# Kernel tuning notes

Hardware: AMD Instinct MI355X
Metric: run time of the kernel (lower is better)

Reference implementation:

```python
import jax, jax.numpy as jnp
import numpy as np


def setup_inputs() -> dict:
    key = jax.random.key(0)
    k1, k2, k3, k4 = jax.random.split(key, 4)
    bs, c, h, w = 8, 64, 64, 64
    x = jax.random.normal(k1, (bs, c, h, w), dtype=jnp.float32)
    # 1x1 conv weights (bias=False): stored as [out_ch, in_ch]
    wq = jax.random.normal(k2, (c // 2, c), dtype=jnp.float32) * (1.0 / np.sqrt(c))
    wk = jax.random.normal(k3, (c // 2, c), dtype=jnp.float32) * (1.0 / np.sqrt(c))
    wv = jax.random.normal(k4, (c, c), dtype=jnp.float32) * (1.0 / np.sqrt(c))
    return {"x": x, "wq": wq, "wk": wk, "wv": wv}


def reference(x, wq, wk, wv):
    bs, c, h, w = x.shape
    hw = h * w
    xf = x.reshape(bs, c, hw)  # [bs, c, hw]
    # 1x1 convs == per-position matmuls
    q = jnp.einsum('dc,bcn->bnd', wq, xf)   # [bs, hw, c//2]
    k = jnp.einsum('dc,bcn->bdn', wk, xf)   # [bs, c//2, hw]
    v = jnp.einsum('dc,bcn->bdn', wv, xf)   # [bs, c,    hw]
    energy = jnp.einsum('bnd,bdm->bnm', q, k)          # [bs, hw, hw]
    attention = jax.nn.softmax(energy, axis=-1)
    # dropout(p=0.1) is identity in eval mode
    out = jnp.einsum('bcm,bnm->bcn', v, attention)      # [bs, c, hw]
    return out.reshape(bs, c, h, w)
```

## Files before the change

### kernel.cpp

```cpp
#include <hip/hip_runtime.h>
#include <hip/hip_fp16.h>


typedef short          f16x8 __attribute__((ext_vector_type(8)));
typedef float          f32x4 __attribute__((ext_vector_type(4)));
typedef unsigned short u16;
typedef unsigned int   u32;

#define HW  4096
#define CC  64
#define DQK 32
#define NBLK2 256
#define THR2 11.54f

__device__ __forceinline__ u16 f2h(float f) {
    __half h = __float2half(f);
    return *reinterpret_cast<u16*>(&h);
}
__device__ __forceinline__ u32 pk2(float a, float b) {
    auto r = __builtin_amdgcn_cvt_pkrtz(a, b);
    u32 u; __builtin_memcpy(&u, &r, 4); return u;
}
__device__ __forceinline__ float ex2(float x) {
    return __builtin_amdgcn_exp2f(x);
}
__device__ __forceinline__ float max16(const f32x4* s) {
    float a = fmaxf(fmaxf(s[0][0], s[0][1]), s[0][2]);
    a = fmaxf(fmaxf(a, s[0][3]), s[1][0]);
    a = fmaxf(fmaxf(a, s[1][1]), s[1][2]);
    a = fmaxf(fmaxf(a, s[1][3]), s[2][0]);
    a = fmaxf(fmaxf(a, s[2][1]), s[2][2]);
    a = fmaxf(fmaxf(a, s[2][3]), s[3][0]);
    a = fmaxf(fmaxf(a, s[3][1]), s[3][2]);
    return fmaxf(a, s[3][3]);
}

__global__ __launch_bounds__(256) void proj_kernel(
    const float* __restrict__ x,  const float* __restrict__ wq,
    const float* __restrict__ wk, const float* __restrict__ wv,
    u16* __restrict__ Qr, u16* __restrict__ Kr, u16* __restrict__ Vc)
{
    const int b   = blockIdx.x;
    const int n0  = blockIdx.y * 64;
    const int tid = threadIdx.x;

    __shared__ __align__(16) u16 Xt[64][88];

    {
        const int c  = tid >> 2;
        const int nc = (tid & 3) * 16;
        const float* src = x + ((size_t)(b * CC + c) * HW + n0 + nc);
        float fv[16];
        *(f32x4*)(fv)      = *(const f32x4*)(src);
        *(f32x4*)(fv + 4)  = *(const f32x4*)(src + 4);
        *(f32x4*)(fv + 8)  = *(const f32x4*)(src + 8);
        *(f32x4*)(fv + 12) = *(const f32x4*)(src + 12);
        #pragma unroll
        for (int i = 0; i < 16; ++i) Xt[nc + i][c] = f2h(fv[i]);
    }
    __syncthreads();

    const int wave = tid >> 6;
    const int lane = tid & 63;
    const int lr   = lane & 15;
    const int lg   = lane >> 4;
    const int lk   = lg * 8;

    const float* W = (wave == 0) ? wq : (wave == 1) ? wk
                   : (wave == 2) ? wv : (wv + 32 * 64);
    const float scale = (wave == 0) ? 1.4426950408889634f : 1.0f;

    f16x8 a[2][2];
    #pragma unroll
    for (int dt = 0; dt < 2; ++dt)
        #pragma unroll
        for (int h = 0; h < 2; ++h) {
            const float* p = W + (dt * 16 + lr) * 64 + h * 32 + lk;
            f32x4 lo = *(const f32x4*)p, hi = *(const f32x4*)(p + 4);
            u16 t[8];
            #pragma unroll
            for (int j = 0; j < 4; ++j) {
                t[j]     = f2h(lo[j] * scale);
                t[4 + j] = f2h(hi[j] * scale);
            }
            a[dt][h] = *(const f16x8*)t;
        }

    const f32x4 fz = {0.f, 0.f, 0.f, 0.f};
    f32x4 acc[2][4];
    #pragma unroll
    for (int dt = 0; dt < 2; ++dt)
        #pragma unroll
        for (int nt = 0; nt < 4; ++nt) acc[dt][nt] = fz;

    #pragma unroll
    for (int nt = 0; nt < 4; ++nt)
        #pragma unroll
        for (int h = 0; h < 2; ++h) {
            f16x8 bx = *(const f16x8*)(&Xt[nt * 16 + lr][h * 32 + lk]);
            #pragma unroll
            for (int dt = 0; dt < 2; ++dt)
                acc[dt][nt] = __builtin_amdgcn_mfma_f32_16x16x32_f16(
                                  a[dt][h], bx, acc[dt][nt], 0, 0, 0);
        }

    if (wave < 2) {
        u16* Out = (wave == 0) ? Qr : Kr;
        #pragma unroll
        for (int dt = 0; dt < 2; ++dt)
            #pragma unroll
            for (int nt = 0; nt < 4; ++nt) {
                const int n = n0 + nt * 16 + lr;
                const int d = dt * 16 + lg * 4;
                u16 pkk[4];
                #pragma unroll
                for (int r = 0; r < 4; ++r) pkk[r] = f2h(acc[dt][nt][r]);
                *(uint2*)(Out + ((size_t)(b * HW + n) * DQK + d)) = *(uint2*)pkk;
            }
    } else {
        const int cbase = (wave - 2) * 32;
        #pragma unroll
        for (int dt = 0; dt < 2; ++dt)
            #pragma unroll
            for (int nt = 0; nt < 4; ++nt) {
                const int m = n0 + nt * 16 + lr;
                #pragma unroll
                for (int r = 0; r < 4; ++r) {
                    const int c = cbase + dt * 16 + lg * 4 + r;
                    Vc[(size_t)(b * CC + c) * HW + m] = f2h(acc[dt][nt][r]);
                }
            }
    }
}

template<int S>
__global__ __launch_bounds__(256, 4) void attn_kernel(
    const u16* __restrict__ Qr, const u16* __restrict__ Kr,
    const u16* __restrict__ Vc, float* __restrict__ out,
    float* __restrict__ Opart, float* __restrict__ Ml)
{
    const int b    = blockIdx.x;
    const int nb   = blockIdx.y;
    const int sp   = blockIdx.z;
    const int n0   = nb * 128;
    const int tid  = threadIdx.x;
    const int wave = tid >> 6;
    const int lane = tid & 63;
    const int lr   = lane & 15;
    const int lg   = lane >> 4;
    const int lk   = lg * 8;

    __shared__ __align__(16) u16 K_lds[2][64 * 40];
    __shared__ __align__(16) u16 V_lds[2][64 * 72];

    const int qb = n0 + wave * 32;
    const f16x8 aq0 = *(const f16x8*)(Qr + (size_t)(b * HW + qb + lr) * DQK + lk);
    const f16x8 aq1 = *(const f16x8*)(Qr + (size_t)(b * HW + qb + 16 + lr) * DQK + lk);

    const f16x8 ones = { 0x3C00, 0x3C00, 0x3C00, 0x3C00,
                         0x3C00, 0x3C00, 0x3C00, 0x3C00 };
    const f32x4 fz = {0.f, 0.f, 0.f, 0.f};

    const int km = tid >> 2, kc = tid & 3;
    const int krow = (km & 32) | (((km >> 2) & 1) << 4)
                   | (((km >> 3) & 3) << 2) | (km & 3);
    const int c0 = tid >> 3, ch = tid & 7;
    const int c1 = 32 + c0;

    const int kvbase = sp * (HW / S);
    const int NT     = HW / S / 64;

    const u16* Kb  = Kr + (size_t)(b * HW + kvbase + km) * DQK + kc * 8;
    const u16* Vb0 = Vc + (size_t)(b * CC + c0) * HW + kvbase + ch * 8;
    const u16* Vb1 = Vc + (size_t)(b * CC + c1) * HW + kvbase + ch * 8;

    f16x8 kreg  = *(const f16x8*)(Kb);
    f16x8 v0reg = *(const f16x8*)(Vb0);
    f16x8 v1reg = *(const f16x8*)(Vb1);
    *(f16x8*)&K_lds[0][krow * 40 + kc * 8] = kreg;
    *(f16x8*)&V_lds[0][c0 * 72 + ch * 8]   = v0reg;
    *(f16x8*)&V_lds[0][c1 * 72 + ch * 8]   = v1reg;
    if (NT > 1) {
        kreg  = *(const f16x8*)(Kb  + (size_t)64 * DQK);
        v0reg = *(const f16x8*)(Vb0 + 64);
        v1reg = *(const f16x8*)(Vb1 + 64);
    }

    f32x4 o[2][4];
    #pragma unroll
    for (int qs = 0; qs < 2; ++qs)
        #pragma unroll
        for (int ct = 0; ct < 4; ++ct) o[qs][ct] = fz;
    f32x4 lrow[2] = {fz, fz};
    float mrow[2] = {-1e30f, -1e30f};

    for (int t = 0; t < NT; ++t) {
        __syncthreads();
        const int cur = t & 1;
        const u16* Kc = K_lds[cur];
        const u16* Vcur = V_lds[cur];

        f32x4 s0[4], s1[4];
        #pragma unroll
        for (int mt = 0; mt < 4; ++mt) {
            f16x8 kf = *(const f16x8*)&Kc[(mt * 16 + lr) * 40 + lk];
            s0[mt] = __builtin_amdgcn_mfma_f32_16x16x32_f16(kf, aq0, fz, 0, 0, 0);
            s1[mt] = __builtin_amdgcn_mfma_f32_16x16x32_f16(kf, aq1, fz, 0, 0, 0);
        }

        if (t + 1 < NT) {
            const int nxt = cur ^ 1;
            *(f16x8*)&K_lds[nxt][krow * 40 + kc * 8] = kreg;
            *(f16x8*)&V_lds[nxt][c0 * 72 + ch * 8]   = v0reg;
            *(f16x8*)&V_lds[nxt][c1 * 72 + ch * 8]   = v1reg;
            if (t + 2 < NT) {
                kreg  = *(const f16x8*)(Kb  + (size_t)(t + 2) * 64 * DQK);
                v0reg = *(const f16x8*)(Vb0 + (t + 2) * 64);
                v1reg = *(const f16x8*)(Vb1 + (t + 2) * 64);
            }
        }

        float lm0 = max16(s0);
        float lm1 = max16(s1);
        if (__any((lm0 > mrow[0] + THR2) | (lm1 > mrow[1] + THR2))) {
            #pragma unroll
            for (int qs = 0; qs < 2; ++qs) {
                float v = qs ? lm1 : lm0;
                v = fmaxf(v, __shfl_xor(v, 16, 64));
                v = fmaxf(v, __shfl_xor(v, 32, 64));
                float mnew  = fmaxf(mrow[qs], v);
                float alpha = ex2(mrow[qs] - mnew);
                mrow[qs] = mnew;
                f32x4 al;
                #pragma unroll
                for (int r = 0; r < 4; ++r) al[r] = __shfl(alpha, 4 * lg + r, 64);
                #pragma unroll
                for (int ct = 0; ct < 4; ++ct)
                    #pragma unroll
                    for (int r = 0; r < 4; ++r) o[qs][ct][r] *= al[r];
                #pragma unroll
                for (int r = 0; r < 4; ++r) lrow[qs][r] *= al[r];
            }
        }

        f16x8 pa[2][2];
        #pragma unroll
        for (int qs = 0; qs < 2; ++qs) {
            const float m = mrow[qs];
            #pragma unroll
            for (int h = 0; h < 2; ++h) {
                u32 w[4];
                #pragma unroll
                for (int half = 0; half < 2; ++half) {
                    const f32x4& sv = qs ? s1[2 * h + half] : s0[2 * h + half];
                    float p0 = ex2(sv[0] - m), p1 = ex2(sv[1] - m);
                    float p2 = ex2(sv[2] - m), p3 = ex2(sv[3] - m);
                    w[2 * half]     = pk2(p0, p1);
                    w[2 * half + 1] = pk2(p2, p3);
                }
                __builtin_memcpy(&pa[qs][h], w, 16);
            }
        }

        #pragma unroll
        for (int qs = 0; qs < 2; ++qs) {
            f32x4 rs = __builtin_amdgcn_mfma_f32_16x16x32_f16(pa[qs][0], ones, fz, 0, 0, 0);
            rs = __builtin_amdgcn_mfma_f32_16x16x32_f16(pa[qs][1], ones, rs, 0, 0, 0);
            #pragma unroll
            for (int r = 0; r < 4; ++r) lrow[qs][r] += rs[r];
        }

        #pragma unroll
        for (int ct = 0; ct < 4; ++ct) {
            const int c = ct * 16 + lr;
            f16x8 bv0 = *(const f16x8*)&Vcur[c * 72 + lk];
            f16x8 bv1 = *(const f16x8*)&Vcur[c * 72 + 32 + lk];
            o[0][ct] = __builtin_amdgcn_mfma_f32_16x16x32_f16(pa[0][0], bv0, o[0][ct], 0, 0, 0);
            o[0][ct] = __builtin_amdgcn_mfma_f32_16x16x32_f16(pa[0][1], bv1, o[0][ct], 0, 0, 0);
            o[1][ct] = __builtin_amdgcn_mfma_f32_16x16x32_f16(pa[1][0], bv0, o[1][ct], 0, 0, 0);
            o[1][ct] = __builtin_amdgcn_mfma_f32_16x16x32_f16(pa[1][1], bv1, o[1][ct], 0, 0, 0);
        }
    }

    if constexpr (S == 1) {
        #pragma unroll
        for (int qs = 0; qs < 2; ++qs)
            #pragma unroll
            for (int ct = 0; ct < 4; ++ct) {
                const int c = ct * 16 + lr;
                f32x4 st;
                #pragma unroll
                for (int r = 0; r < 4; ++r) st[r] = o[qs][ct][r] / lrow[qs][r];
                *(f32x4*)(out + (size_t)(b * CC + c) * HW + qb + qs * 16 + lg * 4) = st;
            }
    } else {
        const int bnb = b * 32 + nb;
        float* Op = Opart + ((size_t)(sp * NBLK2 + bnb) * 64) * 128;
        #pragma unroll
        for (int qs = 0; qs < 2; ++qs)
            #pragma unroll
            for (int ct = 0; ct < 4; ++ct) {
                const int c    = ct * 16 + lr;
                const int qloc = wave * 32 + qs * 16 + lg * 4;
                *(f32x4*)(Op + (size_t)c * 128 + qloc) = o[qs][ct];
            }
        float* Mp = Ml + (size_t)(sp * NBLK2 + bnb) * 256;
        if (lg == 0) {
            Mp[wave * 32 + lr]      = mrow[0];
            Mp[wave * 32 + 16 + lr] = mrow[1];
        }
        if (lr == 0) {
            #pragma unroll
            for (int qs = 0; qs < 2; ++qs)
                #pragma unroll
                for (int r = 0; r < 4; ++r)
                    Mp[128 + wave * 32 + qs * 16 + 4 * lg + r] = lrow[qs][r];
        }
    }
}

template<int S>
__global__ __launch_bounds__(256) void combine_kernel(
    const float* __restrict__ Opart, const float* __restrict__ Ml,
    float* __restrict__ out)
{
    const int bnb = blockIdx.x;
    const int b = bnb >> 5, nb = bnb & 31;
    const int tid = threadIdx.x;
    const int c  = tid >> 2;
    const int q0 = (tid & 3) * 32;

    #pragma unroll
    for (int qq = 0; qq < 32; qq += 4) {
        const int q = q0 + qq;
        f32x4 ms[S], ls[S];
        #pragma unroll
        for (int s = 0; s < S; ++s) {
            const float* Mp = Ml + (size_t)(s * NBLK2 + bnb) * 256;
            ms[s] = *(const f32x4*)(Mp + q);
            ls[s] = *(const f32x4*)(Mp + 128 + q);
        }
        f32x4 M = ms[0];
        #pragma unroll
        for (int s = 1; s < S; ++s)
            #pragma unroll
            for (int j = 0; j < 4; ++j) M[j] = fmaxf(M[j], ms[s][j]);
        f32x4 den = {0.f, 0.f, 0.f, 0.f};
        f32x4 w[S];
        #pragma unroll
        for (int s = 0; s < S; ++s)
            #pragma unroll
            for (int j = 0; j < 4; ++j) {
                w[s][j] = __builtin_amdgcn_exp2f(ms[s][j] - M[j]);
                den[j] += ls[s][j] * w[s][j];
            }
        f32x4 acc = {0.f, 0.f, 0.f, 0.f};
        #pragma unroll
        for (int s = 0; s < S; ++s) {
            f32x4 Ov = *(const f32x4*)(Opart +
                          ((size_t)(s * NBLK2 + bnb) * 64 + c) * 128 + q);
            #pragma unroll
            for (int j = 0; j < 4; ++j) acc[j] += w[s][j] * Ov[j];
        }
        #pragma unroll
        for (int j = 0; j < 4; ++j) acc[j] /= den[j];
        *(f32x4*)(out + (size_t)(b * CC + c) * HW + nb * 128 + q) = acc;
    }
}

extern "C" void kernel_launch(void* const* d_in, const int* in_sizes, int n_in,
                              void* d_out, int out_size, void* d_ws, size_t ws_size,
                              hipStream_t stream)
{
    const float* x  = (const float*)d_in[0];
    const float* wq = (const float*)d_in[1];
    const float* wk = (const float*)d_in[2];
    const float* wv = (const float*)d_in[3];
    u16* ws  = (u16*)d_ws;
    u16* Qr  = ws;
    u16* Kr  = ws + (size_t)8 * HW * DQK;
    u16* Vc  = ws + (size_t)16 * HW * DQK;
    float* Opart = (float*)(ws + (size_t)4194304);
    float* out = (float*)d_out;

    proj_kernel<<<dim3(8, 64), 256, 0, stream>>>(x, wq, wk, wv, Qr, Kr, Vc);

    const size_t qkv_b   = 8ull * 1024 * 1024;
    const size_t opart_b = (size_t)NBLK2 * 64 * 128 * 4;
    const size_t ml_b    = (size_t)NBLK2 * 256 * 4;

    if (ws_size >= qkv_b + 4 * (opart_b + ml_b)) {
        float* Ml = Opart + 4ull * NBLK2 * 64 * 128;
        attn_kernel<4><<<dim3(8, 32, 4), 256, 0, stream>>>(Qr, Kr, Vc, out, Opart, Ml);
        combine_kernel<4><<<NBLK2, 256, 0, stream>>>(Opart, Ml, out);
    } else if (ws_size >= qkv_b + 2 * (opart_b + ml_b)) {
        float* Ml = Opart + 2ull * NBLK2 * 64 * 128;
        attn_kernel<2><<<dim3(8, 32, 2), 256, 0, stream>>>(Qr, Kr, Vc, out, Opart, Ml);
        combine_kernel<2><<<NBLK2, 256, 0, stream>>>(Opart, Ml, out);
    } else {
        attn_kernel<1><<<dim3(8, 32, 1), 256, 0, stream>>>(Qr, Kr, Vc, out, nullptr, nullptr);
    }
}
```

Measured before the change: 74.29 us.

## Store K/V in MFMA fragment order and load directly to registers, drop LDS

The projection kernel now writes K and V in a per-tile layout that matches the MFMA operand fragments. The attention kernel can then load each lane's fragments straight from global memory into registers, which removes the LDS staging, the double buffering and the per-tile __syncthreads. The loop also splits the two query sub-tiles into sequential halves, prefetching the next tile's K and V between them. Partial outputs are normalised and stored as fp16 to halve the combine traffic. The cost is redundant global/L2 loads, since every wave reads the same K/V, and some precision loss in the partials.

```diff
diff --git a/kernel.cpp b/kernel.cpp
--- a/kernel.cpp
+++ b/kernel.cpp
@@ -16,6 +16,9 @@
 __device__ __forceinline__ u16 f2h(float f) {
     __half h = __float2half(f);
     return *reinterpret_cast<u16*>(&h);
+}
+__device__ __forceinline__ float h2f(u16 u) {
+    __half h; __builtin_memcpy(&h, &u, 2); return __half2float(h);
 }
 __device__ __forceinline__ u32 pk2(float a, float b) {
     auto r = __builtin_amdgcn_cvt_pkrtz(a, b);
@@ -38,11 +41,12 @@
 __global__ __launch_bounds__(256) void proj_kernel(
     const float* __restrict__ x,  const float* __restrict__ wq,
     const float* __restrict__ wk, const float* __restrict__ wv,
-    u16* __restrict__ Qr, u16* __restrict__ Kr, u16* __restrict__ Vc)
+    u16* __restrict__ Qr, u16* __restrict__ Kf, u16* __restrict__ Vf)
 {
-    const int b   = blockIdx.x;
-    const int n0  = blockIdx.y * 64;
-    const int tid = threadIdx.x;
+    const int b    = blockIdx.x;
+    const int tile = blockIdx.y;
+    const int n0   = tile * 64;
+    const int tid  = threadIdx.x;
 
     __shared__ __align__(16) u16 Xt[64][88];
 
@@ -104,8 +108,7 @@
                                   a[dt][h], bx, acc[dt][nt], 0, 0, 0);
         }
 
-    if (wave < 2) {
-        u16* Out = (wave == 0) ? Qr : Kr;
+    if (wave == 0) {
         #pragma unroll
         for (int dt = 0; dt < 2; ++dt)
             #pragma unroll
@@ -115,7 +118,23 @@
                 u16 pkk[4];
                 #pragma unroll
                 for (int r = 0; r < 4; ++r) pkk[r] = f2h(acc[dt][nt][r]);
-                *(uint2*)(Out + ((size_t)(b * HW + n) * DQK + d)) = *(uint2*)pkk;
+                *(uint2*)(Qr + ((size_t)(b * HW + n) * DQK + d)) = *(uint2*)pkk;
+            }
+    } else if (wave == 1) {
+        #pragma unroll
+        for (int dt = 0; dt < 2; ++dt)
+            #pragma unroll
+            for (int nt = 0; nt < 4; ++nt) {
+                const int m_in = nt * 16 + lr;
+                const int mt   = 2 * (m_in >> 5) + ((m_in >> 2) & 1);
+                const int lrk  = ((m_in >> 4) & 1) * 8 + ((m_in >> 3) & 1) * 4 + (m_in & 3);
+                const int lgk  = dt * 2 + (lg >> 1);
+                const int j0   = (lg & 1) * 4;
+                u16 pkk[4];
+                #pragma unroll
+                for (int r = 0; r < 4; ++r) pkk[r] = f2h(acc[dt][nt][r]);
+                *(uint2*)(Kf + (size_t)(b * 64 + tile) * 2048
+                             + mt * 512 + lgk * 128 + lrk * 8 + j0) = *(uint2*)pkk;
             }
     } else {
         const int cbase = (wave - 2) * 32;
@@ -123,11 +142,17 @@
         for (int dt = 0; dt < 2; ++dt)
             #pragma unroll
             for (int nt = 0; nt < 4; ++nt) {
-                const int m = n0 + nt * 16 + lr;
+                const int m_in = nt * 16 + lr;
+                const int h    = m_in >> 5;
+                const int lgv  = (m_in >> 3) & 3;
+                const int j    = m_in & 7;
                 #pragma unroll
                 for (int r = 0; r < 4; ++r) {
-                    const int c = cbase + dt * 16 + lg * 4 + r;
-                    Vc[(size_t)(b * CC + c) * HW + m] = f2h(acc[dt][nt][r]);
+                    const int c  = cbase + dt * 16 + lg * 4 + r;
+                    const int ct = c >> 4, lrv = c & 15;
+                    Vf[(size_t)(b * 64 + tile) * 4096
+                       + ct * 1024 + h * 512 + lgv * 128 + lrv * 8 + j]
+                        = f2h(acc[dt][nt][r]);
                 }
             }
     }
@@ -135,14 +160,14 @@
 
 template<int S>
 __global__ __launch_bounds__(256, 4) void attn_kernel(
-    const u16* __restrict__ Qr, const u16* __restrict__ Kr,
-    const u16* __restrict__ Vc, float* __restrict__ out,
-    float* __restrict__ Opart, float* __restrict__ Ml)
+    const u16* __restrict__ Qr, const u16* __restrict__ Kf,
+    const u16* __restrict__ Vf, float* __restrict__ out,
+    u16* __restrict__ Opart, float* __restrict__ Ml)
 {
+    constexpr int NT = HW / S / 64;
     const int b    = blockIdx.x;
     const int nb   = blockIdx.y;
     const int sp   = blockIdx.z;
-    const int n0   = nb * 128;
     const int tid  = threadIdx.x;
     const int wave = tid >> 6;
     const int lane = tid & 63;
@@ -150,10 +175,7 @@
     const int lg   = lane >> 4;
     const int lk   = lg * 8;
 
-    __shared__ __align__(16) u16 K_lds[2][64 * 40];
-    __shared__ __align__(16) u16 V_lds[2][64 * 72];
-
-    const int qb = n0 + wave * 32;
+    const int qb = nb * 128 + wave * 32;
     const f16x8 aq0 = *(const f16x8*)(Qr + (size_t)(b * HW + qb + lr) * DQK + lk);
     const f16x8 aq1 = *(const f16x8*)(Qr + (size_t)(b * HW + qb + 16 + lr) * DQK + lk);
 
@@ -161,30 +183,19 @@
                          0x3C00, 0x3C00, 0x3C00, 0x3C00 };
     const f32x4 fz = {0.f, 0.f, 0.f, 0.f};
 
-    const int km = tid >> 2, kc = tid & 3;
-    const int krow = (km & 32) | (((km >> 2) & 1) << 4)
-                   | (((km >> 3) & 3) << 2) | (km & 3);
-    const int c0 = tid >> 3, ch = tid & 7;
-    const int c1 = 32 + c0;
-
-    const int kvbase = sp * (HW / S);
-    const int NT     = HW / S / 64;
-
-    const u16* Kb  = Kr + (size_t)(b * HW + kvbase + km) * DQK + kc * 8;
-    const u16* Vb0 = Vc + (size_t)(b * CC + c0) * HW + kvbase + ch * 8;
-    const u16* Vb1 = Vc + (size_t)(b * CC + c1) * HW + kvbase + ch * 8;
-
-    f16x8 kreg  = *(const f16x8*)(Kb);
-    f16x8 v0reg = *(const f16x8*)(Vb0);
-    f16x8 v1reg = *(const f16x8*)(Vb1);
-    *(f16x8*)&K_lds[0][krow * 40 + kc * 8] = kreg;
-    *(f16x8*)&V_lds[0][c0 * 72 + ch * 8]   = v0reg;
-    *(f16x8*)&V_lds[0][c1 * 72 + ch * 8]   = v1reg;
-    if (NT > 1) {
-        kreg  = *(const f16x8*)(Kb  + (size_t)64 * DQK);
-        v0reg = *(const f16x8*)(Vb0 + 64);
-        v1reg = *(const f16x8*)(Vb1 + 64);
-    }
+    const int tile0 = sp * NT;
+    const u16* KfT = Kf + (size_t)(b * 64 + tile0) * 2048 + lg * 128 + lr * 8;
+    const u16* VfT = Vf + (size_t)(b * 64 + tile0) * 4096 + lg * 128 + lr * 8;
+
+    f16x8 kf[4], vf[4][2];
+    #pragma unroll
+    for (int mt = 0; mt < 4; ++mt)
+        kf[mt] = *(const f16x8*)(KfT + mt * 512);
+    #pragma unroll
+    for (int ct = 0; ct < 4; ++ct)
+        #pragma unroll
+        for (int h = 0; h < 2; ++h)
+            vf[ct][h] = *(const f16x8*)(VfT + ct * 1024 + h * 512);
 
     f32x4 o[2][4];
     #pragma unroll
@@ -194,92 +205,114 @@
     f32x4 lrow[2] = {fz, fz};
     float mrow[2] = {-1e30f, -1e30f};
 
+    #pragma unroll 2
     for (int t = 0; t < NT; ++t) {
-        __syncthreads();
-        const int cur = t & 1;
-        const u16* Kc = K_lds[cur];
-        const u16* Vcur = V_lds[cur];
-
-        f32x4 s0[4], s1[4];
-        #pragma unroll
-        for (int mt = 0; mt < 4; ++mt) {
-            f16x8 kf = *(const f16x8*)&Kc[(mt * 16 + lr) * 40 + lk];
-            s0[mt] = __builtin_amdgcn_mfma_f32_16x16x32_f16(kf, aq0, fz, 0, 0, 0);
-            s1[mt] = __builtin_amdgcn_mfma_f32_16x16x32_f16(kf, aq1, fz, 0, 0, 0);
-        }
-
-        if (t + 1 < NT) {
-            const int nxt = cur ^ 1;
-            *(f16x8*)&K_lds[nxt][krow * 40 + kc * 8] = kreg;
-            *(f16x8*)&V_lds[nxt][c0 * 72 + ch * 8]   = v0reg;
-            *(f16x8*)&V_lds[nxt][c1 * 72 + ch * 8]   = v1reg;
-            if (t + 2 < NT) {
-                kreg  = *(const f16x8*)(Kb  + (size_t)(t + 2) * 64 * DQK);
-                v0reg = *(const f16x8*)(Vb0 + (t + 2) * 64);
-                v1reg = *(const f16x8*)(Vb1 + (t + 2) * 64);
-            }
-        }
-
-        float lm0 = max16(s0);
-        float lm1 = max16(s1);
-        if (__any((lm0 > mrow[0] + THR2) | (lm1 > mrow[1] + THR2))) {
-            #pragma unroll
-            for (int qs = 0; qs < 2; ++qs) {
-                float v = qs ? lm1 : lm0;
-                v = fmaxf(v, __shfl_xor(v, 16, 64));
-                v = fmaxf(v, __shfl_xor(v, 32, 64));
-                float mnew  = fmaxf(mrow[qs], v);
-                float alpha = ex2(mrow[qs] - mnew);
-                mrow[qs] = mnew;
-                f32x4 al;
-                #pragma unroll
-                for (int r = 0; r < 4; ++r) al[r] = __shfl(alpha, 4 * lg + r, 64);
-                #pragma unroll
-                for (int ct = 0; ct < 4; ++ct)
-                    #pragma unroll
-                    for (int r = 0; r < 4; ++r) o[qs][ct][r] *= al[r];
-                #pragma unroll
-                for (int r = 0; r < 4; ++r) lrow[qs][r] *= al[r];
-            }
-        }
-
-        f16x8 pa[2][2];
-        #pragma unroll
-        for (int qs = 0; qs < 2; ++qs) {
-            const float m = mrow[qs];
+        const int tn = (t + 1 < NT) ? t + 1 : t;
+
+        f32x4 s[4];
+        #pragma unroll
+        for (int mt = 0; mt < 4; ++mt)
+            s[mt] = __builtin_amdgcn_mfma_f32_16x16x32_f16(kf[mt], aq0, fz, 0, 0, 0);
+
+        float lm = max16(s);
+        if (__any(lm > mrow[0] + THR2)) {
+            float v = lm;
+            v = fmaxf(v, __shfl_xor(v, 16, 64));
+            v = fmaxf(v, __shfl_xor(v, 32, 64));
+            float mnew  = fmaxf(mrow[0], v);
+            float alpha = ex2(mrow[0] - mnew);
+            mrow[0] = mnew;
+            f32x4 al;
+            #pragma unroll
+            for (int r = 0; r < 4; ++r) al[r] = __shfl(alpha, 4 * lg + r, 64);
+            #pragma unroll
+            for (int ct = 0; ct < 4; ++ct)
+                #pragma unroll
+                for (int r = 0; r < 4; ++r) o[0][ct][r] *= al[r];
+            #pragma unroll
+            for (int r = 0; r < 4; ++r) lrow[0][r] *= al[r];
+        }
+        f16x8 pa0[2];
+        {
+            const float m = mrow[0];
             #pragma unroll
             for (int h = 0; h < 2; ++h) {
                 u32 w[4];
-                #pragma unroll
-                for (int half = 0; half < 2; ++half) {
-                    const f32x4& sv = qs ? s1[2 * h + half] : s0[2 * h + half];
-                    float p0 = ex2(sv[0] - m), p1 = ex2(sv[1] - m);
-                    float p2 = ex2(sv[2] - m), p3 = ex2(sv[3] - m);
-                    w[2 * half]     = pk2(p0, p1);
-                    w[2 * half + 1] = pk2(p2, p3);
-                }
-                __builtin_memcpy(&pa[qs][h], w, 16);
-            }
-        }
-
-        #pragma unroll
-        for (int qs = 0; qs < 2; ++qs) {
-            f32x4 rs = __builtin_amdgcn_mfma_f32_16x16x32_f16(pa[qs][0], ones, fz, 0, 0, 0);
-            rs = __builtin_amdgcn_mfma_f32_16x16x32_f16(pa[qs][1], ones, rs, 0, 0, 0);
-            #pragma unroll
-            for (int r = 0; r < 4; ++r) lrow[qs][r] += rs[r];
-        }
-
+                w[0] = pk2(ex2(s[2*h][0] - m), ex2(s[2*h][1] - m));
+                w[1] = pk2(ex2(s[2*h][2] - m), ex2(s[2*h][3] - m));
+                w[2] = pk2(ex2(s[2*h+1][0] - m), ex2(s[2*h+1][1] - m));
+                w[3] = pk2(ex2(s[2*h+1][2] - m), ex2(s[2*h+1][3] - m));
+                __builtin_memcpy(&pa0[h], w, 16);
+            }
+        }
+        {
+            f32x4 rs = __builtin_amdgcn_mfma_f32_16x16x32_f16(pa0[0], ones, fz, 0, 0, 0);
+            rs = __builtin_amdgcn_mfma_f32_16x16x32_f16(pa0[1], ones, rs, 0, 0, 0);
+            #pragma unroll
+            for (int r = 0; r < 4; ++r) lrow[0][r] += rs[r];
+        }
         #pragma unroll
         for (int ct = 0; ct < 4; ++ct) {
-            const int c = ct * 16 + lr;
-            f16x8 bv0 = *(const f16x8*)&Vcur[c * 72 + lk];
-            f16x8 bv1 = *(const f16x8*)&Vcur[c * 72 + 32 + lk];
-            o[0][ct] = __builtin_amdgcn_mfma_f32_16x16x32_f16(pa[0][0], bv0, o[0][ct], 0, 0, 0);
-            o[0][ct] = __builtin_amdgcn_mfma_f32_16x16x32_f16(pa[0][1], bv1, o[0][ct], 0, 0, 0);
-            o[1][ct] = __builtin_amdgcn_mfma_f32_16x16x32_f16(pa[1][0], bv0, o[1][ct], 0, 0, 0);
-            o[1][ct] = __builtin_amdgcn_mfma_f32_16x16x32_f16(pa[1][1], bv1, o[1][ct], 0, 0, 0);
-        }
+            o[0][ct] = __builtin_amdgcn_mfma_f32_16x16x32_f16(pa0[0], vf[ct][0], o[0][ct], 0, 0, 0);
+            o[0][ct] = __builtin_amdgcn_mfma_f32_16x16x32_f16(pa0[1], vf[ct][1], o[0][ct], 0, 0, 0);
+        }
+
+        #pragma unroll
+        for (int mt = 0; mt < 4; ++mt)
+            s[mt] = __builtin_amdgcn_mfma_f32_16x16x32_f16(kf[mt], aq1, fz, 0, 0, 0);
+
+        #pragma unroll
+        for (int mt = 0; mt < 4; ++mt)
+            kf[mt] = *(const f16x8*)(KfT + (size_t)tn * 2048 + mt * 512);
+
+        lm = max16(s);
+        if (__any(lm > mrow[1] + THR2)) {
+            float v = lm;
+            v = fmaxf(v, __shfl_xor(v, 16, 64));
+            v = fmaxf(v, __shfl_xor(v, 32, 64));
+            float mnew  = fmaxf(mrow[1], v);
+            float alpha = ex2(mrow[1] - mnew);
+            mrow[1] = mnew;
+            f32x4 al;
+            #pragma unroll
+            for (int r = 0; r < 4; ++r) al[r] = __shfl(alpha, 4 * lg + r, 64);
+            #pragma unroll
+            for (int ct = 0; ct < 4; ++ct)
+                #pragma unroll
+                for (int r = 0; r < 4; ++r) o[1][ct][r] *= al[r];
+            #pragma unroll
+            for (int r = 0; r < 4; ++r) lrow[1][r] *= al[r];
+        }
+        f16x8 pa1[2];
+        {
+            const float m = mrow[1];
+            #pragma unroll
+            for (int h = 0; h < 2; ++h) {
+                u32 w[4];
+                w[0] = pk2(ex2(s[2*h][0] - m), ex2(s[2*h][1] - m));
+                w[1] = pk2(ex2(s[2*h][2] - m), ex2(s[2*h][3] - m));
+                w[2] = pk2(ex2(s[2*h+1][0] - m), ex2(s[2*h+1][1] - m));
+                w[3] = pk2(ex2(s[2*h+1][2] - m), ex2(s[2*h+1][3] - m));
+                __builtin_memcpy(&pa1[h], w, 16);
+            }
+        }
+        {
+            f32x4 rs = __builtin_amdgcn_mfma_f32_16x16x32_f16(pa1[0], ones, fz, 0, 0, 0);
+            rs = __builtin_amdgcn_mfma_f32_16x16x32_f16(pa1[1], ones, rs, 0, 0, 0);
+            #pragma unroll
+            for (int r = 0; r < 4; ++r) lrow[1][r] += rs[r];
+        }
+        #pragma unroll
+        for (int ct = 0; ct < 4; ++ct) {
+            o[1][ct] = __builtin_amdgcn_mfma_f32_16x16x32_f16(pa1[0], vf[ct][0], o[1][ct], 0, 0, 0);
+            o[1][ct] = __builtin_amdgcn_mfma_f32_16x16x32_f16(pa1[1], vf[ct][1], o[1][ct], 0, 0, 0);
+        }
+
+        #pragma unroll
+        for (int ct = 0; ct < 4; ++ct)
+            #pragma unroll
+            for (int h = 0; h < 2; ++h)
+                vf[ct][h] = *(const f16x8*)(VfT + (size_t)tn * 4096 + ct * 1024 + h * 512);
     }
 
     if constexpr (S == 1) {
@@ -295,14 +328,17 @@
             }
     } else {
         const int bnb = b * 32 + nb;
-        float* Op = Opart + ((size_t)(sp * NBLK2 + bnb) * 64) * 128;
+        u16* Op = Opart + ((size_t)(sp * NBLK2 + bnb) * 64) * 128;
         #pragma unroll
         for (int qs = 0; qs < 2; ++qs)
             #pragma unroll
             for (int ct = 0; ct < 4; ++ct) {
                 const int c    = ct * 16 + lr;
                 const int qloc = wave * 32 + qs * 16 + lg * 4;
-                *(f32x4*)(Op + (size_t)c * 128 + qloc) = o[qs][ct];
+                u16 pkk[4];
+                #pragma unroll
+                for (int r = 0; r < 4; ++r) pkk[r] = f2h(o[qs][ct][r] / lrow[qs][r]);
+                *(uint2*)(Op + (size_t)c * 128 + qloc) = *(uint2*)pkk;
             }
         float* Mp = Ml + (size_t)(sp * NBLK2 + bnb) * 256;
         if (lg == 0) {
@@ -321,7 +357,7 @@
 
 template<int S>
 __global__ __launch_bounds__(256) void combine_kernel(
-    const float* __restrict__ Opart, const float* __restrict__ Ml,
+    const u16* __restrict__ Opart, const float* __restrict__ Ml,
     float* __restrict__ out)
 {
     const int bnb = blockIdx.x;
@@ -333,34 +369,38 @@
     #pragma unroll
     for (int qq = 0; qq < 32; qq += 4) {
         const int q = q0 + qq;
-        f32x4 ms[S], ls[S];
+        f32x4 wl[S];
+        f32x4 den = {0.f, 0.f, 0.f, 0.f};
+        f32x4 M;
+        {
+            f32x4 ms[S], ls[S];
+            #pragma unroll
+            for (int s = 0; s < S; ++s) {
+                const float* Mp = Ml + (size_t)(s * NBLK2 + bnb) * 256;
+                ms[s] = *(const f32x4*)(Mp + q);
+                ls[s] = *(const f32x4*)(Mp + 128 + q);
+            }
+            M = ms[0];
+            #pragma unroll
+            for (int s = 1; s < S; ++s)
+                #pragma unroll
+                for (int j = 0; j < 4; ++j) M[j] = fmaxf(M[j], ms[s][j]);
+            #pragma unroll
+            for (int s = 0; s < S; ++s)
+                #pragma unroll
+                for (int j = 0; j < 4; ++j) {
+                    wl[s][j] = ex2(ms[s][j] - M[j]) * ls[s][j];
+                    den[j] += wl[s][j];
+                }
+        }
+        f32x4 acc = {0.f, 0.f, 0.f, 0.f};
         #pragma unroll
         for (int s = 0; s < S; ++s) {
-            const float* Mp = Ml + (size_t)(s * NBLK2 + bnb) * 256;
-            ms[s] = *(const f32x4*)(Mp + q);
-            ls[s] = *(const f32x4*)(Mp + 128 + q);
-        }
-        f32x4 M = ms[0];
-        #pragma unroll
-        for (int s = 1; s < S; ++s)
-            #pragma unroll
-            for (int j = 0; j < 4; ++j) M[j] = fmaxf(M[j], ms[s][j]);
-        f32x4 den = {0.f, 0.f, 0.f, 0.f};
-        f32x4 w[S];
-        #pragma unroll
-        for (int s = 0; s < S; ++s)
-            #pragma unroll
-            for (int j = 0; j < 4; ++j) {
-                w[s][j] = __builtin_amdgcn_exp2f(ms[s][j] - M[j]);
-                den[j] += ls[s][j] * w[s][j];
-            }
-        f32x4 acc = {0.f, 0.f, 0.f, 0.f};
-        #pragma unroll
-        for (int s = 0; s < S; ++s) {
-            f32x4 Ov = *(const f32x4*)(Opart +
+            uint2 hv = *(const uint2*)(Opart +
                           ((size_t)(s * NBLK2 + bnb) * 64 + c) * 128 + q);
-            #pragma unroll
-            for (int j = 0; j < 4; ++j) acc[j] += w[s][j] * Ov[j];
+            u16 h4[4]; __builtin_memcpy(h4, &hv, 8);
+            #pragma unroll
+            for (int j = 0; j < 4; ++j) acc[j] += wl[s][j] * h2f(h4[j]);
         }
         #pragma unroll
         for (int j = 0; j < 4; ++j) acc[j] /= den[j];
@@ -378,26 +418,26 @@
     const float* wv = (const float*)d_in[3];
     u16* ws  = (u16*)d_ws;
     u16* Qr  = ws;
-    u16* Kr  = ws + (size_t)8 * HW * DQK;
-    u16* Vc  = ws + (size_t)16 * HW * DQK;
-    float* Opart = (float*)(ws + (size_t)4194304);
+    u16* Kf  = ws + (size_t)8 * HW * DQK;
+    u16* Vf  = ws + (size_t)16 * HW * DQK;
+    u16* Opart = ws + (size_t)4194304;
     float* out = (float*)d_out;
 
-    proj_kernel<<<dim3(8, 64), 256, 0, stream>>>(x, wq, wk, wv, Qr, Kr, Vc);
+    proj_kernel<<<dim3(8, 64), 256, 0, stream>>>(x, wq, wk, wv, Qr, Kf, Vf);
 
     const size_t qkv_b   = 8ull * 1024 * 1024;
-    const size_t opart_b = (size_t)NBLK2 * 64 * 128 * 4;
+    const size_t opart_b = (size_t)NBLK2 * 64 * 128 * 2;
     const size_t ml_b    = (size_t)NBLK2 * 256 * 4;
 
     if (ws_size >= qkv_b + 4 * (opart_b + ml_b)) {
-        float* Ml = Opart + 4ull * NBLK2 * 64 * 128;
-        attn_kernel<4><<<dim3(8, 32, 4), 256, 0, stream>>>(Qr, Kr, Vc, out, Opart, Ml);
+        float* Ml = (float*)(Opart + 4ull * NBLK2 * 64 * 128);
+        attn_kernel<4><<<dim3(8, 32, 4), 256, 0, stream>>>(Qr, Kf, Vf, out, Opart, Ml);
         combine_kernel<4><<<NBLK2, 256, 0, stream>>>(Opart, Ml, out);
     } else if (ws_size >= qkv_b + 2 * (opart_b + ml_b)) {
-        float* Ml = Opart + 2ull * NBLK2 * 64 * 128;
-        attn_kernel<2><<<dim3(8, 32, 2), 256, 0, stream>>>(Qr, Kr, Vc, out, Opart, Ml);
+        float* Ml = (float*)(Opart + 2ull * NBLK2 * 64 * 128);
+        attn_kernel<2><<<dim3(8, 32, 2), 256, 0, stream>>>(Qr, Kf, Vf, out, Opart, Ml);
         combine_kernel<2><<<NBLK2, 256, 0, stream>>>(Opart, Ml, out);
     } else {
-        attn_kernel<1><<<dim3(8, 32, 1), 256, 0, stream>>>(Qr, Kr, Vc, out, nullptr, nullptr);
-    }
-}
+        attn_kernel<1><<<dim3(8, 32, 1), 256, 0, stream>>>(Qr, Kf, Vf, out, nullptr, nullptr);
+    }
+}
```

Measured after the change: 67.47 us. 1.1x faster.
